# Performance work log

Hardware: AMD Instinct MI355X
Metric: run time of the kernel (lower is better)

## Reference

```python
import jax, jax.numpy as jnp
import numpy as np

N = 4096
CIN = 128
COUT = 128
J = 2
DENSITY = 0.01  # ~40 nonzeros per Laplacian row


def _mask(k):
    m = (jax.random.uniform(k, (N, N)) < DENSITY).astype(jnp.float32)
    # Laplacians have nonzero diagonals; also guarantees no empty softmax rows
    return jnp.maximum(m, jnp.eye(N, dtype=jnp.float32))


def setup_inputs() -> dict:
    key = jax.random.key(0)
    ks = jax.random.split(key, 9)
    x = jax.random.normal(ks[0], (N, CIN), dtype=jnp.float32)
    Lup = _mask(ks[1])
    Ldown = _mask(ks[2])
    P = jax.random.normal(ks[3], (N, N), dtype=jnp.float32) / np.float32(np.sqrt(N))
    weight_irr = jax.random.normal(ks[4], (J, CIN, COUT), dtype=jnp.float32) * 0.05
    weight_sol = jax.random.normal(ks[5], (J, CIN, COUT), dtype=jnp.float32) * 0.05
    weight_har = jax.random.normal(ks[6], (CIN, COUT), dtype=jnp.float32) * 0.05
    att_irr = jax.random.normal(ks[7], (2 * J * COUT, 1), dtype=jnp.float32) * 0.05
    att_sol = jax.random.normal(ks[8], (2 * J * COUT, 1), dtype=jnp.float32) * 0.05
    return {"x": x, "Lup": Lup, "Ldown": Ldown, "P": P,
            "weight_irr": weight_irr, "weight_sol": weight_sol,
            "weight_har": weight_har, "att_irr": att_irr, "att_sol": att_sol}


def _masked_row_softmax(e, mask):
    # torch.sparse.softmax over the mask's nonzero pattern, dim=1, then to_dense
    on = mask > 0
    z = jnp.where(on, e, -jnp.inf)
    m = jnp.max(z, axis=1, keepdims=True)
    m = jnp.where(jnp.isfinite(m), m, 0.0)  # guard fully-masked rows
    p = jnp.exp(z - m)                      # exp(-inf)=0 off-pattern
    s = jnp.sum(p, axis=1, keepdims=True)
    s = jnp.where(s == 0, 1.0, s)
    return jnp.where(on, p / s, 0.0)


def _branch(x, weight, att, mask):
    j, cout = weight.shape[0], weight.shape[2]
    att_slice = j * cout
    h = jnp.einsum('ni,jio->jno', x, weight)         # [J, N, Cout]
    hf = h.reshape(-1, att_slice)                    # [N, J*Cout] (row-major, as torch)
    src = hf @ att[:att_slice]                       # [N, 1]
    dst = hf @ att[att_slice:]                       # [N, 1]
    e = jax.nn.leaky_relu(src + dst.T)               # [N, N], slope 0.01 (torch default)
    alpha = _masked_row_softmax(e, mask)             # [N, N]
    powers = [alpha]
    for _ in range(j - 1):
        powers.append(powers[-1] @ alpha)            # iterative matrix powers
    alpha_exp = jnp.stack(powers)                    # [J, N, N]
    # torch.sum with no dim: full reduction to a SCALAR (faithful to source)
    return jnp.sum(jnp.einsum('jnm,jmo->jno', alpha_exp, h))


def reference(x, Lup, Ldown, P, weight_irr, weight_sol, weight_har, att_irr, att_sol):
    z_irr = _branch(x, weight_irr, att_irr, Ldown)   # scalar
    z_sol = _branch(x, weight_sol, att_sol, Lup)     # scalar
    z_har = (P @ x) @ weight_har                     # [N, Cout]
    return z_irr + z_sol + z_har
```

## Files before the change

kernel.cpp:

```cpp
#include <hip/hip_runtime.h>

typedef __attribute__((ext_vector_type(8))) short short8b;
typedef __attribute__((ext_vector_type(4))) float f32x4;

#define NEG_SENTINEL (-1e30f)

constexpr int C_OFF    = 0;
constexpr int C2_OFF   = 8192;
constexpr int SC_OFF   = 16384;
constexpr int FLAG_I   = 16390;
constexpr int ZERO_N   = 16448;
constexpr int V_OFF    = 16448;
constexpr int NP_OFF   = 19008;
constexpr int SRC_OFF  = 100928;
constexpr int RM_OFF   = 117312;
constexpr int RS_OFF   = 125504;
constexpr int NNZ_OFF  = 133696;
constexpr int CCI_OFF  = 141888;
constexpr int XBT_OFF  = 666176;
constexpr int TP_OFF   = 928320;

__device__ __forceinline__ unsigned short f2bf(float f) {
  unsigned int u = __float_as_uint(f);
  u += 0x7FFFu + ((u >> 16) & 1u);
  return (unsigned short)(u >> 16);
}
__device__ __forceinline__ float bf2f(unsigned short b) {
  return __uint_as_float(((unsigned int)b) << 16);
}
__device__ __forceinline__ float scrub(float v) {
  unsigned int u = __float_as_uint(v);
  return ((u & 0x7F800000u) == 0x7F800000u) ? 0.f : v;
}

__global__ __launch_bounds__(128) void k_vvec(const void* __restrict__ xin,
                                              const void* __restrict__ w_irr,
                                              const void* __restrict__ w_sol,
                                              const void* __restrict__ att_irr,
                                              const void* __restrict__ att_sol,
                                              int* __restrict__ flagp,
                                              float* __restrict__ vvec) {
  __shared__ int sdet[128];
  int t = threadIdx.x;
  unsigned int ef = (((const unsigned int*)xin)[t] >> 7) & 0xFFu;
  sdet[t] = (ef >= 100u && ef <= 150u) ? 1 : 0;
  __syncthreads();
  for (int d = 64; d > 0; d >>= 1) { if (t < d) sdet[t] += sdet[t + d]; __syncthreads(); }
  int f = (sdet[0] >= 96) ? 1 : 0;
  if (blockIdx.x == 0 && t == 0) *flagp = f;
  int bx = blockIdx.x;
  int b = bx / 10, rem = bx % 10, j = rem / 5, tt = rem % 5;
  const void* Wv = (b == 0 ? w_irr : w_sol);
  const void* Av = (b == 0 ? att_irr : att_sol);
  int i = t;
  float s = 0.f;
  if (f) {
    const unsigned short* Wr = (const unsigned short*)Wv + (size_t)j * 16384 + (size_t)i * 128;
    const unsigned short* Ar = (const unsigned short*)Av + tt * 128;
    for (int o = 0; o < 128; o += 8) {
      uint4 wq = *(const uint4*)(Wr + o);
      unsigned int ww[4] = {wq.x, wq.y, wq.z, wq.w};
      float cf[8];
      if (tt < 4) {
        uint4 aq = *(const uint4*)(Ar + o);
        unsigned int aa[4] = {aq.x, aq.y, aq.z, aq.w};
#pragma unroll
        for (int u = 0; u < 4; ++u) {
          cf[2 * u] = bf2f((unsigned short)(aa[u] & 0xFFFFu));
          cf[2 * u + 1] = bf2f((unsigned short)(aa[u] >> 16));
        }
      } else {
#pragma unroll
        for (int e = 0; e < 8; ++e) cf[e] = 1.0f;
      }
#pragma unroll
      for (int u = 0; u < 4; ++u) {
        s += bf2f((unsigned short)(ww[u] & 0xFFFFu)) * cf[2 * u];
        s += bf2f((unsigned short)(ww[u] >> 16)) * cf[2 * u + 1];
      }
    }
  } else {
    const float* Wr = (const float*)Wv + (size_t)j * 16384 + (size_t)i * 128;
    const float* Ar = (const float*)Av + tt * 128;
    for (int o = 0; o < 128; o += 4) {
      float4 wq = *(const float4*)(Wr + o);
      float4 aq = {1.f, 1.f, 1.f, 1.f};
      if (tt < 4) aq = *(const float4*)(Ar + o);
      s += wq.x * aq.x + wq.y * aq.y + wq.z * aq.z + wq.w * aq.w;
    }
  }
  vvec[bx * 128 + i] = s;
}

__global__ __launch_bounds__(256) void k_prep(const void* __restrict__ xin,
                                              const int* __restrict__ flag,
                                              const float* __restrict__ vvec,
                                              unsigned short* __restrict__ xbT,
                                              float* __restrict__ np,
                                              float* __restrict__ srcdst) {
  __shared__ __align__(16) float ldsx[64 * 130];
  __shared__ __align__(16) float ldsv[2560];
  __shared__ float ldsp[4 * 1280];
  __shared__ float npl[1280];
  int f = *flag;
  int t = threadIdx.x, nb = blockIdx.x * 64;
  for (int q = 0; q < 16; ++q) {
    int idx = q * 256 + t;
    int row = idx >> 6, cp = idx & 63;
    float vx, vy;
    if (f) {
      unsigned int u = ((const unsigned int*)xin)[(size_t)(nb + row) * 64 + cp];
      vx = bf2f((unsigned short)(u & 0xFFFFu));
      vy = bf2f((unsigned short)(u >> 16));
    } else {
      float2 v = ((const float2*)xin)[(size_t)(nb + row) * 64 + cp];
      vx = v.x; vy = v.y;
    }
    ldsx[row * 130 + cp * 2] = vx;
    ldsx[row * 130 + cp * 2 + 1] = vy;
  }
  for (int q = 0; q < 10; ++q) { int idx = q * 256 + t; ldsv[idx] = vvec[idx]; }
  __syncthreads();
  for (int q = 0; q < 32; ++q) {
    int idx = q * 256 + t;
    int c = idx >> 6, n = idx & 63;
    xbT[(size_t)c * 4096 + nb + n] = f2bf(ldsx[n * 130 + c]);
  }
  int row = t & 63, qq = t >> 6, i0 = qq * 32;
  float acc[20];
#pragma unroll
  for (int k = 0; k < 20; ++k) acc[k] = 0.f;
  for (int i = i0; i < i0 + 32; i += 2) {
    float2 xv = *(const float2*)&ldsx[row * 130 + i];
#pragma unroll
    for (int k = 0; k < 20; ++k) {
      float2 vk = *(const float2*)&ldsv[k * 128 + i];
      acc[k] += xv.x * vk.x + xv.y * vk.y;
    }
  }
#pragma unroll
  for (int k = 0; k < 20; ++k) ldsp[qq * 1280 + row * 20 + k] = acc[k];
  __syncthreads();
  for (int rep = 0; rep < 5; ++rep) {
    int idx = rep * 256 + t;
    int k = idx >> 6, rr = idx & 63;
    float s = ldsp[rr * 20 + k] + ldsp[1280 + rr * 20 + k] +
              ldsp[2560 + rr * 20 + k] + ldsp[3840 + rr * 20 + k];
    npl[k * 64 + rr] = s;
    np[(size_t)k * 4096 + nb + rr] = s;
  }
  __syncthreads();
  {
    int b = t >> 7, j = (t >> 6) & 1, kind = (t >> 5) & 1, q = t & 31;
    int bl = q * 2;
    int r = j * 2048 + (nb >> 1) + q;
    int kidx = b * 10 + j * 5 + kind * 2;
    float val = npl[kidx * 64 + bl] + npl[(kidx + 1) * 64 + bl + 1];
    srcdst[b * 8192 + kind * 4096 + r] = val;
  }
}

__device__ __forceinline__ int col_of(int f, int l, int bit) {
  if (f) return ((bit >> 3) * 512) + l * 8 + (bit & 7);
  return ((bit >> 5) * 2048) + (((bit >> 2) & 7) * 256) + l * 4 + (bit & 3);
}

__global__ __launch_bounds__(256) void k_scan(const void* __restrict__ Ldown,
                                              const void* __restrict__ Lup,
                                              float* __restrict__ ws) {
  int b = blockIdx.y, t = threadIdx.x;
  int wid = t >> 6, l = t & 63;
  int r = blockIdx.x * 4 + wid;
  int f = ((const int*)ws)[FLAG_I];
  unsigned short* cci = (unsigned short*)(ws + CCI_OFF) + (size_t)(b * 4096 + r) * 128;
  unsigned long long hm = 0ULL;
  if (f) {
    const uint4* rp = (const uint4*)((const unsigned short*)(b ? Lup : Ldown) +
                                     (size_t)r * 4096) + l;
    uint4 cs[8];
#pragma unroll
    for (int it = 0; it < 8; ++it) cs[it] = rp[it * 64];
#pragma unroll
    for (int it = 0; it < 8; ++it) {
      unsigned int wv[4] = {cs[it].x, cs[it].y, cs[it].z, cs[it].w};
#pragma unroll
      for (int u = 0; u < 4; ++u) {
        hm |= ((unsigned long long)((wv[u] & 0xFFFFu) != 0u)) << (it * 8 + u * 2);
        hm |= ((unsigned long long)((wv[u] >> 16) != 0u)) << (it * 8 + u * 2 + 1);
      }
    }
  } else {
    const uint4* rp = (const uint4*)((const float*)(b ? Lup : Ldown) +
                                     (size_t)r * 4096) + l;
#pragma unroll
    for (int p = 0; p < 2; ++p) {
      uint4 cs[8];
#pragma unroll
      for (int it = 0; it < 8; ++it) cs[it] = rp[(p * 8 + it) * 64];
#pragma unroll
      for (int it = 0; it < 8; ++it) {
        unsigned int wv[4] = {cs[it].x, cs[it].y, cs[it].z, cs[it].w};
#pragma unroll
        for (int u = 0; u < 4; ++u)
          hm |= ((unsigned long long)(wv[u] != 0u)) << (p * 32 + it * 4 + u);
      }
    }
  }
  int cnt = __popcll(hm);
  int pre = cnt;
  for (int d = 1; d < 64; d <<= 1) {
    int o = __shfl_up(pre, d);
    if (l >= d) pre += o;
  }
  int base = pre - cnt;
  int nz = __shfl(pre, 63);
  if (l == 0) ((int*)ws)[NNZ_OFF + b * 4096 + r] = min(nz, 128);
  const float* srcp = ws + SRC_OFF + b * 8192;
  const float* dstp = srcp + 4096;
  float srcr = srcp[r];
  float mx = NEG_SENTINEL, sm = 0.f;
  unsigned long long mm = hm;
  while (mm) {
    int bit = __builtin_ctzll(mm); mm &= mm - 1;
    int m = col_of(f, l, bit);
    float e = srcr + dstp[m];
    e = (e >= 0.f) ? e : 0.01f * e;
    if (e > mx) { sm = sm * __expf(mx - e) + 1.f; mx = e; }
    else        { sm += __expf(e - mx); }
  }
  for (int d = 1; d < 64; d <<= 1) {
    float om = __shfl_xor(mx, d);
    float os = __shfl_xor(sm, d);
    float M = fmaxf(mx, om);
    sm = sm * __expf(mx - M) + os * __expf(om - M);
    mx = M;
  }
  if (l == 0) {
    ws[RM_OFF + b * 4096 + r] = mx;
    ws[RS_OFF + b * 4096 + r] = sm;
  }
  float inv = 1.0f / sm;
  int slot = base;
  mm = hm;
  while (mm) {
    int bit = __builtin_ctzll(mm); mm &= mm - 1;
    int m = col_of(f, l, bit);
    if (slot < 128) cci[slot] = (unsigned short)m;
    ++slot;
    float e = srcr + dstp[m];
    e = (e >= 0.f) ? e : 0.01f * e;
    atomicAdd(&ws[C_OFF + b * 4096 + m], __expf(e - mx) * inv);
  }
}

__device__ __forceinline__ float alpha_of(const float* ws, int b, int r, int m) {
  const float* srcp = ws + SRC_OFF + b * 8192;
  float e = srcp[r] + srcp[4096 + m];
  e = (e >= 0.f) ? e : 0.01f * e;
  return __expf(e - ws[RM_OFF + b * 4096 + r]) / ws[RS_OFF + b * 4096 + r];
}

__global__ __launch_bounds__(256) void k_c2(float* __restrict__ ws) {
  int b = blockIdx.y;
  int s = blockIdx.x * 256 + threadIdx.x;
  int r = s >> 7, k = s & 127;
  int nz = ((const int*)ws)[NNZ_OFF + b * 4096 + r];
  if (k < nz) {
    int m = ((const unsigned short*)(ws + CCI_OFF))[(size_t)(b * 4096 + r) * 128 + k];
    atomicAdd(&ws[C2_OFF + b * 4096 + m], ws[C_OFF + b * 4096 + r] * alpha_of(ws, b, r, m));
  }
}

__global__ __launch_bounds__(256) void k_scalar(float* __restrict__ ws) {
  int b = blockIdx.x, t = threadIdx.x;
  const float* cb  = ws + C_OFF  + b * 4096;
  const float* c2b = ws + C2_OFF + b * 4096;
  const float* hr0 = ws + NP_OFF + (b * 10 + 4) * 4096;
  const float* hr1 = ws + NP_OFF + (b * 10 + 9) * 4096;
  double acc = 0.0;
  for (int m = t; m < 4096; m += 256)
    acc += (double)scrub(cb[m]) * (double)scrub(hr0[m]) +
           (double)scrub(c2b[m]) * (double)scrub(hr1[m]);
  __shared__ double sd[256];
  sd[t] = acc;
  __syncthreads();
  for (int s = 128; s > 0; s >>= 1) { if (t < s) sd[t] += sd[t + s]; __syncthreads(); }
  if (t == 0) atomicAdd(&ws[SC_OFF], (float)sd[0]);
}

__global__ __launch_bounds__(256) void k_gemm1(const void* __restrict__ P,
                                               const unsigned short* __restrict__ xbT,
                                               const int* __restrict__ flag,
                                               float* __restrict__ TP) {
  __shared__ __align__(16) unsigned short a_lds[64 * 40];
  __shared__ __align__(16) unsigned short b_lds[128 * 40];
  int f = *flag;
  const int mt = blockIdx.x & 63, ks = blockIdx.x >> 6;
  const int mb = mt * 64;
  const int t = threadIdx.x;
  const int w = t >> 6, l = t & 63, quad = l >> 4, lr = l & 15;
  f32x4 acc[8] = {};
  const int arow = t >> 2, akq = (t & 3) << 3;
  const int bn = t >> 1, bh = (t & 1) << 4;
  const int k0 = ks * 512;
  uint4 aU, bU0, bU1;
#define LOADT(IT)                                                              \
  {                                                                            \
    const int kb = k0 + (IT) * 32;                                             \
    if (f) {                                                                   \
      aU = *(const uint4*)((const unsigned short*)P +                          \
                           (size_t)(mb + arow) * 4096 + kb + akq);             \
    } else {                                                                   \
      const float* pa = (const float*)P + (size_t)(mb + arow) * 4096 + kb + akq; \
      float4 f0 = *(const float4*)pa;                                          \
      float4 f1 = *(const float4*)(pa + 4);                                    \
      unsigned short u[8] = {f2bf(f0.x), f2bf(f0.y), f2bf(f0.z), f2bf(f0.w),   \
                             f2bf(f1.x), f2bf(f1.y), f2bf(f1.z), f2bf(f1.w)};  \
      aU = *(const uint4*)u;                                                   \
    }                                                                          \
    const unsigned short* src = xbT + (size_t)bn * 4096 + kb + bh;             \
    bU0 = *(const uint4*)src;                                                  \
    bU1 = *(const uint4*)(src + 8);                                            \
  }
  LOADT(0);
  for (int it = 0; it < 16; ++it) {
    *(uint4*)&a_lds[arow * 40 + akq] = aU;
    *(uint4*)&b_lds[bn * 40 + bh] = bU0;
    *(uint4*)&b_lds[bn * 40 + bh + 8] = bU1;
    __syncthreads();
    if (it < 15) LOADT(it + 1);
    short8b af = *(short8b*)&a_lds[(w * 16 + lr) * 40 + quad * 8];
#pragma unroll
    for (int nt = 0; nt < 8; ++nt) {
      short8b bf = *(short8b*)&b_lds[(nt * 16 + lr) * 40 + quad * 8];
      acc[nt] = __builtin_amdgcn_mfma_f32_16x16x32_bf16(af, bf, acc[nt], 0, 0, 0);
    }
    if (it < 15) __syncthreads();
  }
#undef LOADT
  float* Tp = TP + (size_t)ks * 524288;
#pragma unroll
  for (int nt = 0; nt < 8; ++nt)
#pragma unroll
    for (int rr = 0; rr < 4; ++rr) {
      int row = mb + w * 16 + quad * 4 + rr;
      int col = nt * 16 + lr;
      Tp[(size_t)row * 128 + col] = acc[nt][rr];
    }
}

__global__ __launch_bounds__(256) void k_gemm2(const float* __restrict__ TP,
                                               const void* __restrict__ W,
                                               const float* __restrict__ ws,
                                               void* __restrict__ outv) {
  __shared__ float tl[16 * 128];
  int f = ((const int*)ws)[FLAG_I];
  int t = threadIdx.x;
  int rb = blockIdx.x * 16;
  for (int q = 0; q < 2; ++q) {
    int vi = q * 256 + t;
    size_t base = (size_t)rb * 128 + (size_t)vi * 4;
    float4 s = {0.f, 0.f, 0.f, 0.f};
#pragma unroll
    for (int p = 0; p < 8; ++p) {
      float4 v = *(const float4*)&TP[(size_t)p * 524288 + base];
      s.x += v.x; s.y += v.y; s.z += v.z; s.w += v.w;
    }
    *(float4*)&tl[vi * 4] = s;
  }
  __syncthreads();
  int col = t & 127, rg = t >> 7;
  int r0 = rg * 8;
  float acc[8] = {};
  for (int k = 0; k < 128; k += 4) {
    float w0, w1, w2, w3;
    if (f) {
      const unsigned short* W16 = (const unsigned short*)W;
      w0 = bf2f(W16[(k + 0) * 128 + col]); w1 = bf2f(W16[(k + 1) * 128 + col]);
      w2 = bf2f(W16[(k + 2) * 128 + col]); w3 = bf2f(W16[(k + 3) * 128 + col]);
    } else {
      const float* W32 = (const float*)W;
      w0 = W32[(k + 0) * 128 + col]; w1 = W32[(k + 1) * 128 + col];
      w2 = W32[(k + 2) * 128 + col]; w3 = W32[(k + 3) * 128 + col];
    }
#pragma unroll
    for (int rr = 0; rr < 8; ++rr) {
      float4 tv = *(const float4*)&tl[(r0 + rr) * 128 + k];
      acc[rr] += tv.x * w0 + tv.y * w1 + tv.z * w2 + tv.w * w3;
    }
  }
  float s = scrub(ws[SC_OFF]);
#pragma unroll
  for (int rr = 0; rr < 8; ++rr) {
    size_t oi = (size_t)(rb + r0 + rr) * 128 + col;
    float v = s + acc[rr];
    if (f) ((unsigned short*)outv)[oi] = f2bf(v);
    else   ((float*)outv)[oi] = v;
  }
}

extern "C" void kernel_launch(void* const* d_in, const int* in_sizes, int n_in,
                              void* d_out, int out_size, void* d_ws, size_t ws_size,
                              hipStream_t stream) {
  const void* x       = d_in[0];
  const void* Lup     = d_in[1];
  const void* Ldown   = d_in[2];
  const void* P       = d_in[3];
  const void* w_irr   = d_in[4];
  const void* w_sol   = d_in[5];
  const void* w_har   = d_in[6];
  const void* att_irr = d_in[7];
  const void* att_sol = d_in[8];
  float* ws = (float*)d_ws;

  hipMemsetAsync(d_ws, 0, (size_t)ZERO_N * sizeof(float), stream);
  k_vvec  <<<20, 128, 0, stream>>>(x, w_irr, w_sol, att_irr, att_sol,
                                   (int*)ws + FLAG_I, ws + V_OFF);
  k_prep  <<<64, 256, 0, stream>>>(x, (int*)ws + FLAG_I, ws + V_OFF,
                                   (unsigned short*)(ws + XBT_OFF), ws + NP_OFF,
                                   ws + SRC_OFF);
  k_gemm1 <<<512, 256, 0, stream>>>(P, (const unsigned short*)(ws + XBT_OFF),
                                    (int*)ws + FLAG_I, ws + TP_OFF);
  k_scan  <<<dim3(1024, 2), 256, 0, stream>>>(Ldown, Lup, ws);
  k_c2    <<<dim3(2048, 2), 256, 0, stream>>>(ws);
  k_scalar<<<2, 256, 0, stream>>>(ws);
  k_gemm2 <<<256, 256, 0, stream>>>(ws + TP_OFF, w_har, ws, d_out);
}
```

Baseline: 306.7 us.

## Split mask scan into bitmap-building kernel and softmax kernel over contiguous columns

```diff
diff --git a/kernel.cpp b/kernel.cpp
--- a/kernel.cpp
+++ b/kernel.cpp
@@ -19,6 +19,7 @@
 constexpr int CCI_OFF  = 141888;
 constexpr int XBT_OFF  = 666176;
 constexpr int TP_OFF   = 928320;
+constexpr int BM_OFF   = 5122624;
 
 __device__ __forceinline__ unsigned short f2bf(float f) {
   unsigned int u = __float_as_uint(f);
@@ -160,52 +161,41 @@
   }
 }
 
-__device__ __forceinline__ int col_of(int f, int l, int bit) {
-  if (f) return ((bit >> 3) * 512) + l * 8 + (bit & 7);
-  return ((bit >> 5) * 2048) + (((bit >> 2) & 7) * 256) + l * 4 + (bit & 3);
-}
-
-__global__ __launch_bounds__(256) void k_scan(const void* __restrict__ Ldown,
+__global__ __launch_bounds__(256) void k_mask(const void* __restrict__ Ldown,
                                               const void* __restrict__ Lup,
-                                              float* __restrict__ ws) {
+                                              const int* __restrict__ flag,
+                                              unsigned char* __restrict__ bm) {
+  int f = *flag;
+  int b = blockIdx.y;
+  const void* mask = b ? Lup : Ldown;
+  int idx = blockIdx.x * 256 + threadIdx.x;
+  unsigned int byte = 0;
+  if (f) {
+    uint4 v = ((const uint4*)mask)[idx];
+    unsigned int wv[4] = {v.x, v.y, v.z, v.w};
+#pragma unroll
+    for (int u = 0; u < 4; ++u) {
+      byte |= ((wv[u] & 0xFFFFu) != 0u ? 1u : 0u) << (2 * u);
+      byte |= ((wv[u] >> 16) != 0u ? 1u : 0u) << (2 * u + 1);
+    }
+  } else {
+    const uint4* p = (const uint4*)mask + (size_t)idx * 2;
+    uint4 v0 = p[0], v1 = p[1];
+    unsigned int wv[8] = {v0.x, v0.y, v0.z, v0.w, v1.x, v1.y, v1.z, v1.w};
+#pragma unroll
+    for (int u = 0; u < 8; ++u) byte |= (wv[u] != 0u ? 1u : 0u) << u;
+  }
+  bm[(size_t)b * 2097152 + idx] = (unsigned char)byte;
+}
+
+__global__ __launch_bounds__(256) void k_soft(float* __restrict__ ws) {
+  const unsigned char* bm = (const unsigned char*)(ws + BM_OFF);
   int b = blockIdx.y, t = threadIdx.x;
   int wid = t >> 6, l = t & 63;
   int r = blockIdx.x * 4 + wid;
-  int f = ((const int*)ws)[FLAG_I];
   unsigned short* cci = (unsigned short*)(ws + CCI_OFF) + (size_t)(b * 4096 + r) * 128;
-  unsigned long long hm = 0ULL;
-  if (f) {
-    const uint4* rp = (const uint4*)((const unsigned short*)(b ? Lup : Ldown) +
-                                     (size_t)r * 4096) + l;
-    uint4 cs[8];
-#pragma unroll
-    for (int it = 0; it < 8; ++it) cs[it] = rp[it * 64];
-#pragma unroll
-    for (int it = 0; it < 8; ++it) {
-      unsigned int wv[4] = {cs[it].x, cs[it].y, cs[it].z, cs[it].w};
-#pragma unroll
-      for (int u = 0; u < 4; ++u) {
-        hm |= ((unsigned long long)((wv[u] & 0xFFFFu) != 0u)) << (it * 8 + u * 2);
-        hm |= ((unsigned long long)((wv[u] >> 16) != 0u)) << (it * 8 + u * 2 + 1);
-      }
-    }
-  } else {
-    const uint4* rp = (const uint4*)((const float*)(b ? Lup : Ldown) +
-                                     (size_t)r * 4096) + l;
-#pragma unroll
-    for (int p = 0; p < 2; ++p) {
-      uint4 cs[8];
-#pragma unroll
-      for (int it = 0; it < 8; ++it) cs[it] = rp[(p * 8 + it) * 64];
-#pragma unroll
-      for (int it = 0; it < 8; ++it) {
-        unsigned int wv[4] = {cs[it].x, cs[it].y, cs[it].z, cs[it].w};
-#pragma unroll
-        for (int u = 0; u < 4; ++u)
-          hm |= ((unsigned long long)(wv[u] != 0u)) << (p * 32 + it * 4 + u);
-      }
-    }
-  }
+  unsigned long long hm =
+      ((const unsigned long long*)(bm + ((size_t)b * 4096 + r) * 512))[l];
   int cnt = __popcll(hm);
   int pre = cnt;
   for (int d = 1; d < 64; d <<= 1) {
@@ -218,13 +208,17 @@
   const float* srcp = ws + SRC_OFF + b * 8192;
   const float* dstp = srcp + 4096;
   float srcr = srcp[r];
+  float ev[6];
+  int nh = 0;
   float mx = NEG_SENTINEL, sm = 0.f;
   unsigned long long mm = hm;
   while (mm) {
     int bit = __builtin_ctzll(mm); mm &= mm - 1;
-    int m = col_of(f, l, bit);
+    int m = l * 64 + bit;
     float e = srcr + dstp[m];
     e = (e >= 0.f) ? e : 0.01f * e;
+    if (nh < 6) ev[nh] = e;
+    ++nh;
     if (e > mx) { sm = sm * __expf(mx - e) + 1.f; mx = e; }
     else        { sm += __expf(e - mx); }
   }
@@ -240,15 +234,17 @@
     ws[RS_OFF + b * 4096 + r] = sm;
   }
   float inv = 1.0f / sm;
-  int slot = base;
+  int slot = base, i = 0;
   mm = hm;
   while (mm) {
     int bit = __builtin_ctzll(mm); mm &= mm - 1;
-    int m = col_of(f, l, bit);
+    int m = l * 64 + bit;
     if (slot < 128) cci[slot] = (unsigned short)m;
     ++slot;
-    float e = srcr + dstp[m];
-    e = (e >= 0.f) ? e : 0.01f * e;
+    float e;
+    if (i < 6) e = ev[i];
+    else { e = srcr + dstp[m]; e = (e >= 0.f) ? e : 0.01f * e; }
+    ++i;
     atomicAdd(&ws[C_OFF + b * 4096 + m], __expf(e - mx) * inv);
   }
 }
@@ -421,7 +417,9 @@
                                    ws + SRC_OFF);
   k_gemm1 <<<512, 256, 0, stream>>>(P, (const unsigned short*)(ws + XBT_OFF),
                                     (int*)ws + FLAG_I, ws + TP_OFF);
-  k_scan  <<<dim3(1024, 2), 256, 0, stream>>>(Ldown, Lup, ws);
+  k_mask  <<<dim3(8192, 2), 256, 0, stream>>>(Ldown, Lup, (int*)ws + FLAG_I,
+                                              (unsigned char*)(ws + BM_OFF));
+  k_soft  <<<dim3(1024, 2), 256, 0, stream>>>(ws);
   k_c2    <<<dim3(2048, 2), 256, 0, stream>>>(ws);
   k_scalar<<<2, 256, 0, stream>>>(ws);
   k_gemm2 <<<256, 256, 0, stream>>>(ws + TP_OFF, w_har, ws, d_out);
```

Result: slower. 322.0 us (+5.0%).
